# Performance work log

Hardware: AMD Instinct MI355X
Metric: run time of the kernel (lower is better)

Reference implementation:

```python
import jax, jax.numpy as jnp
import numpy as np

SEQ = 2048
HID = 4096
N_HEADS = 32
N_KV = 8
HEAD_DIM = 128
EPS = 1e-6


def _rope_tables(max_pos, dim, base=10000.0):
    inv_freq = 1.0 / (base ** (np.arange(0, dim, 2, dtype=np.float32) / dim))
    t = np.arange(max_pos, dtype=np.float32)
    freqs = np.outer(t, inv_freq)                     # [P, D/2]
    emb = np.concatenate([freqs, freqs], axis=-1)     # [P, D]
    return jnp.asarray(np.cos(emb)), jnp.asarray(np.sin(emb))


def setup_inputs() -> dict:
    key = jax.random.key(0)
    ks = jax.random.split(key, 6)
    s = 0.02
    cos, sin = _rope_tables(SEQ, HEAD_DIM)
    causal = jnp.tril(jnp.ones((SEQ, SEQ), dtype=bool))
    attn_mask = jnp.where(causal, 0.0, -1e9).astype(jnp.float32)
    return {
        "x": jax.random.normal(ks[0], (SEQ, HID), dtype=jnp.float32),
        "position_ids": jnp.arange(SEQ, dtype=jnp.int32),
        "cos": cos,
        "sin": sin,
        "attn_mask": attn_mask,
        "Wq": jax.random.normal(ks[1], (HID, N_HEADS * HEAD_DIM), dtype=jnp.float32) * s,
        "Wk": jax.random.normal(ks[2], (HID, N_KV * HEAD_DIM), dtype=jnp.float32) * s,
        "Wv": jax.random.normal(ks[3], (HID, N_KV * HEAD_DIM), dtype=jnp.float32) * s,
        "Wo": jax.random.normal(ks[4], (N_HEADS * HEAD_DIM, HID), dtype=jnp.float32) * s,
        "q_norm_w": jnp.ones((HEAD_DIM,), dtype=jnp.float32),
        "k_norm_w": jnp.ones((HEAD_DIM,), dtype=jnp.float32),
    }


def _rms_norm(x, w):
    # x: [H, S, D]; normalize over last dim
    return w * (x * jax.lax.rsqrt(jnp.mean(x * x, axis=-1, keepdims=True) + EPS))


def _apply_rope(x, cos, sin, position_ids):
    # x: [H, S, D]; cos/sin: [P, D]
    c = cos[position_ids][None]  # [1, S, D]
    s = sin[position_ids][None]
    half = x.shape[-1] // 2
    x1, x2 = x[..., :half], x[..., half:]
    rotated = jnp.concatenate([-x2, x1], axis=-1)
    return x * c + rotated * s


def reference(x, position_ids, cos, sin, attn_mask, Wq, Wk, Wv, Wo, q_norm_w, k_norm_w):
    S = x.shape[0]
    q = (x @ Wq).reshape(S, N_HEADS, HEAD_DIM).transpose(1, 0, 2)   # [H, S, D]
    k = (x @ Wk).reshape(S, N_KV, HEAD_DIM).transpose(1, 0, 2)      # [Hkv, S, D]
    v = (x @ Wv).reshape(S, N_KV, HEAD_DIM).transpose(1, 0, 2)
    q = _rms_norm(q, q_norm_w)
    k = _rms_norm(k, k_norm_w)
    q = _apply_rope(q, cos, sin, position_ids)
    k = _apply_rope(k, cos, sin, position_ids)
    # GQA: repeat_interleave kv heads to match q heads
    groups = N_HEADS // N_KV
    k = jnp.repeat(k, groups, axis=0)  # [H, S, D]
    v = jnp.repeat(v, groups, axis=0)
    scores = jnp.einsum("hqd,hkd->hqk", q, k) * (HEAD_DIM ** -0.5)
    scores = scores + attn_mask  # broadcast [S,S] -> [H,S,S]
    attn = jax.nn.softmax(scores.astype(jnp.float32), axis=-1).astype(x.dtype)
    out = jnp.einsum("hqk,hkd->hqd", attn, v)   # [H, S, D]
    out = out.transpose(1, 0, 2).reshape(S, N_HEADS * HEAD_DIM)
    return out @ Wo
```

## Files before the change

### kernel.cpp

```cpp
#include <hip/hip_runtime.h>

typedef unsigned short u16;
typedef __attribute__((ext_vector_type(8))) short bf16x8;
typedef __attribute__((ext_vector_type(4))) float f32x4;

__device__ __forceinline__ float bf2f(u16 b) {
    unsigned int u = ((unsigned int)b) << 16;
    float f;
    __builtin_memcpy(&f, &u, 4);
    return f;
}
__device__ __forceinline__ u16 f2bf(float f) {
    unsigned int u;
    __builtin_memcpy(&u, &f, 4);
    unsigned int r = u + 0x7FFFu + ((u >> 16) & 1u);
    return (u16)(r >> 16);
}

__device__ __forceinline__ void async_copy16(const void* g, void* lds) {
    __builtin_amdgcn_global_load_lds(
        (const __attribute__((address_space(1))) unsigned int*)g,
        (__attribute__((address_space(3))) unsigned int*)lds, 16, 0, 0);
}

#define MFMA(a, b, c) __builtin_amdgcn_mfma_f32_16x16x32_bf16((a), (b), (c), 0, 0, 0)

__global__ __launch_bounds__(256) void cvt_f32_bf16(
    const float* __restrict__ src, u16* __restrict__ dst)
{
    int i = (blockIdx.x * 256 + threadIdx.x) * 8;
    float4 a = *(const float4*)(src + i);
    float4 b = *(const float4*)(src + i + 4);
    uint4 o;
    u16* po = (u16*)&o;
    po[0] = f2bf(a.x); po[1] = f2bf(a.y); po[2] = f2bf(a.z); po[3] = f2bf(a.w);
    po[4] = f2bf(b.x); po[5] = f2bf(b.y); po[6] = f2bf(b.z); po[7] = f2bf(b.w);
    *(uint4*)(dst + i) = o;
}

__global__ __launch_bounds__(256) void transpose_cvt(
    const float* __restrict__ src, u16* __restrict__ dst, int R, int C)
{
    __shared__ u16 T[64][65];
    int r0 = blockIdx.y * 64, c0 = blockIdx.x * 64;
    int t = threadIdx.x;
#pragma unroll
    for (int i = 0; i < 4; ++i) {
        int c = i * 256 + t;
        int row = c >> 4, col4 = (c & 15) * 4;
        float4 v = *(const float4*)(src + (size_t)(r0 + row) * C + c0 + col4);
        T[row][col4 + 0] = f2bf(v.x);
        T[row][col4 + 1] = f2bf(v.y);
        T[row][col4 + 2] = f2bf(v.z);
        T[row][col4 + 3] = f2bf(v.w);
    }
    __syncthreads();
#pragma unroll
    for (int i = 0; i < 2; ++i) {
        int c = i * 256 + t;
        int row = c >> 3, col8 = (c & 7) * 8;
        uint4 o;
        u16* po = (u16*)&o;
#pragma unroll
        for (int j = 0; j < 8; ++j) po[j] = T[col8 + j][row];
        *(uint4*)(dst + (size_t)(c0 + row) * R + r0 + col8) = o;
    }
}

template <bool F32OUT>
__global__ __launch_bounds__(256) void gemm_bt(
    const u16* __restrict__ A, const u16* __restrict__ Bt, void* __restrict__ Cp,
    int M, int N, int K)
{
    __shared__ u16 As[128][64];
    __shared__ u16 Bs[128][64];
    int tid = threadIdx.x;
    int w = tid >> 6, lane = tid & 63;
    int quad = lane >> 4, l15 = lane & 15;
    int m0 = blockIdx.y * 128, n0 = blockIdx.x * 128;
    int wm = w >> 1, wn = w & 1;

    f32x4 acc[4][4] = {};

    for (int k0 = 0; k0 < K; k0 += 64) {
#pragma unroll
        for (int i = 0; i < 4; ++i) {
            int row = w * 32 + i * 8 + (lane >> 3);
            int s = lane & 7;
            int gc = s ^ (row & 7);
            async_copy16(A + (size_t)(m0 + row) * K + k0 + gc * 8, &As[w * 32 + i * 8][0]);
            async_copy16(Bt + (size_t)(n0 + row) * K + k0 + gc * 8, &Bs[w * 32 + i * 8][0]);
        }
        __syncthreads();
#pragma unroll
        for (int kk = 0; kk < 2; ++kk) {
            bf16x8 a[4], b[4];
            int kq = kk * 4 + quad;
#pragma unroll
            for (int mt = 0; mt < 4; ++mt) {
                int m = wm * 64 + mt * 16 + l15;
                a[mt] = *(const bf16x8*)&As[m][(kq ^ (m & 7)) * 8];
            }
#pragma unroll
            for (int nt = 0; nt < 4; ++nt) {
                int n = wn * 64 + nt * 16 + l15;
                b[nt] = *(const bf16x8*)&Bs[n][(kq ^ (n & 7)) * 8];
            }
#pragma unroll
            for (int mt = 0; mt < 4; ++mt)
#pragma unroll
                for (int nt = 0; nt < 4; ++nt)
                    acc[mt][nt] = MFMA(a[mt], b[nt], acc[mt][nt]);
        }
        __syncthreads();
    }

#pragma unroll
    for (int mt = 0; mt < 4; ++mt)
#pragma unroll
        for (int nt = 0; nt < 4; ++nt)
#pragma unroll
            for (int r = 0; r < 4; ++r) {
                int m = m0 + wm * 64 + mt * 16 + quad * 4 + r;
                int n = n0 + wn * 64 + nt * 16 + l15;
                if (F32OUT)
                    ((float*)Cp)[(size_t)m * N + n] = acc[mt][nt][r];
                else
                    ((u16*)Cp)[(size_t)m * N + n] = f2bf(acc[mt][nt][r]);
            }
}

__global__ __launch_bounds__(256) void norm_rope(
    const u16* __restrict__ QKV, const int* __restrict__ pos,
    const float* __restrict__ cosT, const float* __restrict__ sinT,
    const float* __restrict__ qw, const float* __restrict__ kw,
    u16* __restrict__ Qr, u16* __restrict__ Kr)
{
    int gw = blockIdx.x * 4 + (threadIdx.x >> 6);
    int lane = threadIdx.x & 63;
    int s = gw / 40;
    int hh = gw - s * 40;
    bool isq = hh < 32;
    int h = isq ? hh : hh - 32;
    int col0 = isq ? h * 128 : 4096 + h * 128;
    const u16* x = QKV + (size_t)s * 6144 + col0;
    float x1 = bf2f(x[lane]);
    float x2 = bf2f(x[lane + 64]);
    float ss = x1 * x1 + x2 * x2;
#pragma unroll
    for (int m = 1; m < 64; m <<= 1) ss += __shfl_xor(ss, m);
    float r = rsqrtf(ss * (1.0f / 128.0f) + 1e-6f);
    const float* wgt = isq ? qw : kw;
    float y1 = x1 * r * wgt[lane];
    float y2 = x2 * r * wgt[lane + 64];
    int p = pos[s];
    float c1 = cosT[p * 128 + lane], c2 = cosT[p * 128 + lane + 64];
    float s1 = sinT[p * 128 + lane], s2 = sinT[p * 128 + lane + 64];
    float o1 = y1 * c1 - y2 * s1;
    float o2 = y2 * c2 + y1 * s2;
    u16* dst = (isq ? Qr : Kr) + ((size_t)h * 2048 + s) * 128;
    dst[lane] = f2bf(o1);
    dst[lane + 64] = f2bf(o2);
}

__global__ __launch_bounds__(256) void v_transpose(
    const u16* __restrict__ QKV, u16* __restrict__ Vt)
{
    __shared__ u16 T[64][130];
    int s0 = blockIdx.x * 64;
    int kh = blockIdx.y;
    int t = threadIdx.x;
#pragma unroll
    for (int i = 0; i < 4; ++i) {
        int c = i * 256 + t;
        int srow = c >> 4, d8 = (c & 15) * 8;
        uint4 v = *(const uint4*)(QKV + (size_t)(s0 + srow) * 6144 + 5120 + kh * 128 + d8);
        const u16* pv = (const u16*)&v;
#pragma unroll
        for (int j = 0; j < 8; ++j) T[srow][d8 + j] = pv[j];
    }
    __syncthreads();
#pragma unroll
    for (int i = 0; i < 4; ++i) {
        int c = i * 256 + t;
        int drow = c >> 3, s8 = (c & 7) * 8;
        uint4 o;
        u16* po = (u16*)&o;
#pragma unroll
        for (int j = 0; j < 8; ++j) po[j] = T[s8 + j][drow];
        *(uint4*)(Vt + ((size_t)kh * 128 + drow) * 2048 + s0 + s8) = o;
    }
}

__global__ __launch_bounds__(256) void flash_attn(
    const u16* __restrict__ Qr, const u16* __restrict__ Kr,
    const u16* __restrict__ Vt, u16* __restrict__ O)
{
    __shared__ u16 Ks[64][128];
    __shared__ u16 Vs[128][64];
    __shared__ u16 Ps[4][16][72];

    int h = blockIdx.y;
    int qi = blockIdx.x;
    int tid = threadIdx.x;
    int w = tid >> 6, lane = tid & 63;
    int quad = lane >> 4, l15 = lane & 15;
    int kvh = h >> 2;
    int q0 = qi * 64;

    bf16x8 qf[4];
    const u16* qbase = Qr + ((size_t)h * 2048 + q0 + w * 16 + l15) * 128;
#pragma unroll
    for (int kk = 0; kk < 4; ++kk)
        qf[kk] = *(const bf16x8*)(qbase + kk * 32 + quad * 8);

    float m_i[4], l_i[4];
#pragma unroll
    for (int r = 0; r < 4; ++r) { m_i[r] = -__builtin_inff(); l_i[r] = 0.0f; }
    f32x4 acc_o[8] = {};

    const float scale = 0.08838834764831845f;
    const float L2E = 1.44269504f;

    for (int kt = 0; kt <= qi; ++kt) {
        int k0 = kt * 64;
#pragma unroll
        for (int i = 0; i < 4; ++i) {
            int c = (w * 4 + i) * 64 + lane;
            int krow = c >> 4, ks = c & 15;
            int kgc = ks ^ (krow & 7);
            async_copy16(Kr + ((size_t)kvh * 2048 + k0 + krow) * 128 + kgc * 8,
                         &Ks[(w * 4 + i) * 4][0]);
            int vrow = c >> 3, vs = c & 7;
            int vgc = vs ^ (vrow & 7);
            async_copy16(Vt + ((size_t)kvh * 128 + vrow) * 2048 + k0 + vgc * 8,
                         &Vs[(w * 4 + i) * 8][0]);
        }
        __syncthreads();

        f32x4 sa[4] = {};
#pragma unroll
        for (int nt = 0; nt < 4; ++nt) {
            int krow = nt * 16 + l15;
#pragma unroll
            for (int kk = 0; kk < 4; ++kk) {
                int kq = kk * 4 + quad;
                bf16x8 kf = *(const bf16x8*)&Ks[krow][(kq ^ (krow & 7)) * 8];
                sa[nt] = MFMA(qf[kk], kf, sa[nt]);
            }
        }

        bool diag = (kt == qi);
        float sv[4][4], pv[4][4], mloc[4];
#pragma unroll
        for (int r = 0; r < 4; ++r) mloc[r] = -__builtin_inff();
#pragma unroll
        for (int nt = 0; nt < 4; ++nt)
#pragma unroll
            for (int r = 0; r < 4; ++r) {
                float v = sa[nt][r] * scale;
                if (diag) {
                    int key = k0 + nt * 16 + l15;
                    int qrow = q0 + w * 16 + quad * 4 + r;
                    if (key > qrow) v = -__builtin_inff();
                }
                sv[nt][r] = v;
                mloc[r] = fmaxf(mloc[r], v);
            }
#pragma unroll
        for (int r = 0; r < 4; ++r) {
#pragma unroll
            for (int m = 1; m < 16; m <<= 1) mloc[r] = fmaxf(mloc[r], __shfl_xor(mloc[r], m));
        }
        float alpha[4];
#pragma unroll
        for (int r = 0; r < 4; ++r) {
            float mnew = fmaxf(m_i[r], mloc[r]);
            alpha[r] = exp2f((m_i[r] - mnew) * L2E);
            m_i[r] = mnew;
            float rs = 0.0f;
#pragma unroll
            for (int nt = 0; nt < 4; ++nt) {
                float p = exp2f((sv[nt][r] - mnew) * L2E);
                pv[nt][r] = p;
                rs += p;
            }
#pragma unroll
            for (int m = 1; m < 16; m <<= 1) rs += __shfl_xor(rs, m);
            l_i[r] = l_i[r] * alpha[r] + rs;
        }
#pragma unroll
        for (int nt = 0; nt < 8; ++nt)
#pragma unroll
            for (int r = 0; r < 4; ++r) acc_o[nt][r] *= alpha[r];

#pragma unroll
        for (int nt = 0; nt < 4; ++nt)
#pragma unroll
            for (int r = 0; r < 4; ++r)
                Ps[w][quad * 4 + r][nt * 16 + l15] = f2bf(pv[nt][r]);
        asm volatile("s_waitcnt lgkmcnt(0)" ::: "memory");

        bf16x8 pf[2];
#pragma unroll
        for (int kk = 0; kk < 2; ++kk)
            pf[kk] = *(const bf16x8*)&Ps[w][l15][kk * 32 + quad * 8];

#pragma unroll
        for (int nt = 0; nt < 8; ++nt) {
            int vrow = nt * 16 + l15;
#pragma unroll
            for (int kk = 0; kk < 2; ++kk) {
                int kq = kk * 4 + quad;
                bf16x8 vf = *(const bf16x8*)&Vs[vrow][(kq ^ (vrow & 7)) * 8];
                acc_o[nt] = MFMA(pf[kk], vf, acc_o[nt]);
            }
        }
        __syncthreads();
    }

#pragma unroll
    for (int nt = 0; nt < 8; ++nt)
#pragma unroll
        for (int r = 0; r < 4; ++r) {
            int qrow = q0 + w * 16 + quad * 4 + r;
            int d = nt * 16 + l15;
            O[(size_t)qrow * 4096 + h * 128 + d] = f2bf(acc_o[nt][r] / l_i[r]);
        }
}

extern "C" void kernel_launch(void* const* d_in, const int* in_sizes, int n_in,
                              void* d_out, int out_size, void* d_ws, size_t ws_size,
                              hipStream_t stream) {
    const float* x    = (const float*)d_in[0];
    const int*   pos  = (const int*)d_in[1];
    const float* cosT = (const float*)d_in[2];
    const float* sinT = (const float*)d_in[3];
    const float* Wq = (const float*)d_in[5];
    const float* Wk = (const float*)d_in[6];
    const float* Wv = (const float*)d_in[7];
    const float* Wo = (const float*)d_in[8];
    const float* qw = (const float*)d_in[9];
    const float* kw = (const float*)d_in[10];
    float* out = (float*)d_out;

    char* ws = (char*)d_ws;
    u16* WT  = (u16*)ws;
    u16* QKV = (u16*)(ws + 50331648ull);
    u16* Qr  = (u16*)(ws + 75497472ull);
    u16* Kr  = (u16*)(ws + 92274688ull);
    u16* Vt  = (u16*)(ws + 96468992ull);
    u16* Xb  = (u16*)(ws + 100663296ull);
    u16* AttnOut = QKV;

    dim3 blk(256);
    cvt_f32_bf16<<<dim3(4096), blk, 0, stream>>>(x, Xb);
    transpose_cvt<<<dim3(64, 64), blk, 0, stream>>>(Wq, WT, 4096, 4096);
    transpose_cvt<<<dim3(16, 64), blk, 0, stream>>>(Wk, WT + 4096ull * 4096, 4096, 1024);
    transpose_cvt<<<dim3(16, 64), blk, 0, stream>>>(Wv, WT + 5120ull * 4096, 4096, 1024);
    gemm_bt<false><<<dim3(48, 16), blk, 0, stream>>>(Xb, WT, QKV, 2048, 6144, 4096);
    norm_rope<<<dim3(20480), blk, 0, stream>>>(QKV, pos, cosT, sinT, qw, kw, Qr, Kr);
    v_transpose<<<dim3(32, 8), blk, 0, stream>>>(QKV, Vt);
    transpose_cvt<<<dim3(64, 64), blk, 0, stream>>>(Wo, WT, 4096, 4096);
    flash_attn<<<dim3(32, 32), blk, 0, stream>>>(Qr, Kr, Vt, AttnOut);
    gemm_bt<true><<<dim3(32, 16), blk, 0, stream>>>(AttnOut, WT, out, 2048, 4096, 4096);
}
```

Baseline: 626.5 us.

## Share K/V tiles across GQA heads and double-buffer flash attention loads

The attention kernel is restructured so each block handles one KV head with its four query heads (one per wave), each wave taking 32 query rows. One K/V tile staged in LDS is therefore reused by all four query heads. K/V loads are double-buffered so the next tile's async copy overlaps compute, and the block order is remapped to pair short and long causal tiles. This cuts redundant K/V global traffic and sync stalls, but raises register and LDS use per block, which could lower occupancy.

Result: faster. 552.4 us (-11.8%).

```diff
diff --git a/kernel.cpp b/kernel.cpp
--- a/kernel.cpp
+++ b/kernel.cpp
@@ -192,141 +192,179 @@
     }
 }
 
-__global__ __launch_bounds__(256) void flash_attn(
+__global__ __launch_bounds__(256, 2) void flash_attn2(
     const u16* __restrict__ Qr, const u16* __restrict__ Kr,
     const u16* __restrict__ Vt, u16* __restrict__ O)
 {
-    __shared__ u16 Ks[64][128];
-    __shared__ u16 Vs[128][64];
-    __shared__ u16 Ps[4][16][72];
-
-    int h = blockIdx.y;
-    int qi = blockIdx.x;
+    __shared__ u16 Ks[2][64][128];
+    __shared__ u16 Vs[2][128][64];
+    __shared__ u16 Ps[4][32][64];
+
+    int f = blockIdx.x + 64 * blockIdx.y;
+    int lo = f & 255, hi = f >> 8;
+    int qt  = hi ? 63 - (lo & 63) : (lo & 63);
+    int kvh = (lo >> 6) + hi * 4;
+
     int tid = threadIdx.x;
     int w = tid >> 6, lane = tid & 63;
     int quad = lane >> 4, l15 = lane & 15;
-    int kvh = h >> 2;
-    int q0 = qi * 64;
-
-    bf16x8 qf[4];
-    const u16* qbase = Qr + ((size_t)h * 2048 + q0 + w * 16 + l15) * 128;
-#pragma unroll
-    for (int kk = 0; kk < 4; ++kk)
-        qf[kk] = *(const bf16x8*)(qbase + kk * 32 + quad * 8);
-
-    float m_i[4], l_i[4];
-#pragma unroll
-    for (int r = 0; r < 4; ++r) { m_i[r] = -__builtin_inff(); l_i[r] = 0.0f; }
-    f32x4 acc_o[8] = {};
+    int h = kvh * 4 + w;
+    int q0 = qt * 32;
+    int nkt = qt / 2 + 1;
+
+    bf16x8 qf[2][4];
+#pragma unroll
+    for (int mt = 0; mt < 2; ++mt) {
+        const u16* qb = Qr + ((size_t)h * 2048 + q0 + mt * 16 + l15) * 128;
+#pragma unroll
+        for (int kk = 0; kk < 4; ++kk)
+            qf[mt][kk] = *(const bf16x8*)(qb + kk * 32 + quad * 8);
+    }
+
+    float m_i[8], l_i[8];
+#pragma unroll
+    for (int r = 0; r < 8; ++r) { m_i[r] = -__builtin_inff(); l_i[r] = 0.0f; }
+    f32x4 acc[2][8] = {};
 
     const float scale = 0.08838834764831845f;
     const float L2E = 1.44269504f;
 
-    for (int kt = 0; kt <= qi; ++kt) {
+    auto stage = [&](int kt, int b) {
         int k0 = kt * 64;
 #pragma unroll
         for (int i = 0; i < 4; ++i) {
-            int c = (w * 4 + i) * 64 + lane;
-            int krow = c >> 4, ks = c & 15;
-            int kgc = ks ^ (krow & 7);
-            async_copy16(Kr + ((size_t)kvh * 2048 + k0 + krow) * 128 + kgc * 8,
-                         &Ks[(w * 4 + i) * 4][0]);
-            int vrow = c >> 3, vs = c & 7;
-            int vgc = vs ^ (vrow & 7);
-            async_copy16(Vt + ((size_t)kvh * 128 + vrow) * 2048 + k0 + vgc * 8,
-                         &Vs[(w * 4 + i) * 8][0]);
-        }
+            int idx = (w * 4 + i) * 64 + lane;
+            int krow = idx >> 4, kp = idx & 15;
+            int kg = (kp & 8) | ((kp ^ krow) & 7);
+            async_copy16(Kr + ((size_t)kvh * 2048 + k0 + krow) * 128 + kg * 8,
+                         &Ks[b][(w * 4 + i) * 4][0]);
+            int vrow = idx >> 3, vp = idx & 7;
+            int vg = vp ^ (vrow & 7);
+            async_copy16(Vt + ((size_t)kvh * 128 + vrow) * 2048 + k0 + vg * 8,
+                         &Vs[b][(w * 4 + i) * 8][0]);
+        }
+    };
+
+    stage(0, 0);
+
+    for (int kt = 0; kt < nkt; ++kt) {
+        int b = kt & 1;
+        int k0 = kt * 64;
         __syncthreads();
-
-        f32x4 sa[4] = {};
+        if (kt + 1 < nkt) stage(kt + 1, b ^ 1);
+
+        f32x4 sa[2][4] = {};
 #pragma unroll
         for (int nt = 0; nt < 4; ++nt) {
             int krow = nt * 16 + l15;
 #pragma unroll
             for (int kk = 0; kk < 4; ++kk) {
                 int kq = kk * 4 + quad;
-                bf16x8 kf = *(const bf16x8*)&Ks[krow][(kq ^ (krow & 7)) * 8];
-                sa[nt] = MFMA(qf[kk], kf, sa[nt]);
-            }
-        }
-
-        bool diag = (kt == qi);
-        float sv[4][4], pv[4][4], mloc[4];
-#pragma unroll
-        for (int r = 0; r < 4; ++r) mloc[r] = -__builtin_inff();
-#pragma unroll
-        for (int nt = 0; nt < 4; ++nt)
+                int kph = (kq & 8) | ((kq ^ krow) & 7);
+                bf16x8 kf = *(const bf16x8*)&Ks[b][krow][kph * 8];
+                sa[0][nt] = MFMA(qf[0][kk], kf, sa[0][nt]);
+                sa[1][nt] = MFMA(qf[1][kk], kf, sa[1][nt]);
+            }
+        }
+
+        bool last = (kt == nkt - 1);
+        float pv[2][4][4], mloc[8];
+#pragma unroll
+        for (int r = 0; r < 8; ++r) mloc[r] = -__builtin_inff();
+#pragma unroll
+        for (int mt = 0; mt < 2; ++mt)
+#pragma unroll
+            for (int nt = 0; nt < 4; ++nt)
+#pragma unroll
+                for (int r = 0; r < 4; ++r) {
+                    float v = sa[mt][nt][r] * scale;
+                    if (last) {
+                        int key = k0 + nt * 16 + l15;
+                        int qrow = q0 + mt * 16 + quad * 4 + r;
+                        if (key > qrow) v = -__builtin_inff();
+                    }
+                    pv[mt][nt][r] = v;
+                    mloc[mt * 4 + r] = fmaxf(mloc[mt * 4 + r], v);
+                }
+#pragma unroll
+        for (int r = 0; r < 8; ++r)
+#pragma unroll
+            for (int m = 1; m < 16; m <<= 1)
+                mloc[r] = fmaxf(mloc[r], __shfl_xor(mloc[r], m));
+
+        float alpha[8];
+#pragma unroll
+        for (int mt = 0; mt < 2; ++mt)
 #pragma unroll
             for (int r = 0; r < 4; ++r) {
-                float v = sa[nt][r] * scale;
-                if (diag) {
-                    int key = k0 + nt * 16 + l15;
-                    int qrow = q0 + w * 16 + quad * 4 + r;
-                    if (key > qrow) v = -__builtin_inff();
+                int rr = mt * 4 + r;
+                float mnew = fmaxf(m_i[rr], mloc[rr]);
+                alpha[rr] = exp2f((m_i[rr] - mnew) * L2E);
+                m_i[rr] = mnew;
+                float rs = 0.0f;
+#pragma unroll
+                for (int nt = 0; nt < 4; ++nt) {
+                    float p = exp2f((pv[mt][nt][r] - mnew) * L2E);
+                    pv[mt][nt][r] = p;
+                    rs += p;
                 }
-                sv[nt][r] = v;
-                mloc[r] = fmaxf(mloc[r], v);
-            }
-#pragma unroll
-        for (int r = 0; r < 4; ++r) {
-#pragma unroll
-            for (int m = 1; m < 16; m <<= 1) mloc[r] = fmaxf(mloc[r], __shfl_xor(mloc[r], m));
-        }
-        float alpha[4];
-#pragma unroll
-        for (int r = 0; r < 4; ++r) {
-            float mnew = fmaxf(m_i[r], mloc[r]);
-            alpha[r] = exp2f((m_i[r] - mnew) * L2E);
-            m_i[r] = mnew;
-            float rs = 0.0f;
-#pragma unroll
-            for (int nt = 0; nt < 4; ++nt) {
-                float p = exp2f((sv[nt][r] - mnew) * L2E);
-                pv[nt][r] = p;
-                rs += p;
-            }
-#pragma unroll
-            for (int m = 1; m < 16; m <<= 1) rs += __shfl_xor(rs, m);
-            l_i[r] = l_i[r] * alpha[r] + rs;
-        }
-#pragma unroll
-        for (int nt = 0; nt < 8; ++nt)
-#pragma unroll
-            for (int r = 0; r < 4; ++r) acc_o[nt][r] *= alpha[r];
-
-#pragma unroll
-        for (int nt = 0; nt < 4; ++nt)
-#pragma unroll
-            for (int r = 0; r < 4; ++r)
-                Ps[w][quad * 4 + r][nt * 16 + l15] = f2bf(pv[nt][r]);
+#pragma unroll
+                for (int m = 1; m < 16; m <<= 1) rs += __shfl_xor(rs, m);
+                l_i[rr] = l_i[rr] * alpha[rr] + rs;
+            }
+#pragma unroll
+        for (int mt = 0; mt < 2; ++mt)
+#pragma unroll
+            for (int nt = 0; nt < 8; ++nt)
+#pragma unroll
+                for (int r = 0; r < 4; ++r) acc[mt][nt][r] *= alpha[mt * 4 + r];
+
+#pragma unroll
+        for (int mt = 0; mt < 2; ++mt)
+#pragma unroll
+            for (int nt = 0; nt < 4; ++nt)
+#pragma unroll
+                for (int r = 0; r < 4; ++r) {
+                    int row = mt * 16 + quad * 4 + r;
+                    int col = nt * 16 + l15;
+                    int ph = ((col >> 3) ^ (row & 7)) * 8 + (col & 7);
+                    Ps[w][row][ph] = f2bf(pv[mt][nt][r]);
+                }
         asm volatile("s_waitcnt lgkmcnt(0)" ::: "memory");
 
-        bf16x8 pf[2];
-#pragma unroll
-        for (int kk = 0; kk < 2; ++kk)
-            pf[kk] = *(const bf16x8*)&Ps[w][l15][kk * 32 + quad * 8];
+        bf16x8 pf[2][2];
+#pragma unroll
+        for (int mt = 0; mt < 2; ++mt) {
+            int row = mt * 16 + l15;
+#pragma unroll
+            for (int kk = 0; kk < 2; ++kk)
+                pf[mt][kk] = *(const bf16x8*)&Ps[w][row][((kk * 4 + quad) ^ (row & 7)) * 8];
+        }
 
 #pragma unroll
         for (int nt = 0; nt < 8; ++nt) {
             int vrow = nt * 16 + l15;
 #pragma unroll
             for (int kk = 0; kk < 2; ++kk) {
-                int kq = kk * 4 + quad;
-                bf16x8 vf = *(const bf16x8*)&Vs[vrow][(kq ^ (vrow & 7)) * 8];
-                acc_o[nt] = MFMA(pf[kk], vf, acc_o[nt]);
-            }
-        }
-        __syncthreads();
-    }
-
-#pragma unroll
-    for (int nt = 0; nt < 8; ++nt)
-#pragma unroll
-        for (int r = 0; r < 4; ++r) {
-            int qrow = q0 + w * 16 + quad * 4 + r;
-            int d = nt * 16 + l15;
-            O[(size_t)qrow * 4096 + h * 128 + d] = f2bf(acc_o[nt][r] / l_i[r]);
-        }
+                int vph = (kk * 4 + quad) ^ (vrow & 7);
+                bf16x8 vf = *(const bf16x8*)&Vs[b][vrow][vph * 8];
+                acc[0][nt] = MFMA(pf[0][kk], vf, acc[0][nt]);
+                acc[1][nt] = MFMA(pf[1][kk], vf, acc[1][nt]);
+            }
+        }
+    }
+
+#pragma unroll
+    for (int mt = 0; mt < 2; ++mt)
+#pragma unroll
+        for (int nt = 0; nt < 8; ++nt)
+#pragma unroll
+            for (int r = 0; r < 4; ++r) {
+                int qrow = q0 + mt * 16 + quad * 4 + r;
+                int d = nt * 16 + l15;
+                O[(size_t)qrow * 4096 + h * 128 + d] =
+                    f2bf(acc[mt][nt][r] / l_i[mt * 4 + r]);
+            }
 }
 
 extern "C" void kernel_launch(void* const* d_in, const int* in_sizes, int n_in,
@@ -362,6 +400,6 @@
     norm_rope<<<dim3(20480), blk, 0, stream>>>(QKV, pos, cosT, sinT, qw, kw, Qr, Kr);
     v_transpose<<<dim3(32, 8), blk, 0, stream>>>(QKV, Vt);
     transpose_cvt<<<dim3(64, 64), blk, 0, stream>>>(Wo, WT, 4096, 4096);
-    flash_attn<<<dim3(32, 32), blk, 0, stream>>>(Qr, Kr, Vt, AttnOut);
+    flash_attn2<<<dim3(64, 8), blk, 0, stream>>>(Qr, Kr, Vt, AttnOut);
     gemm_bt<true><<<dim3(32, 16), blk, 0, stream>>>(AttnOut, WT, out, 2048, 4096, 4096);
 }
```
